# Kernel optimization log

Hardware: AMD Instinct MI355X
Metric: run time of the kernel (lower is better)

The kernel has to match this reference:

```python
import jax, jax.numpy as jnp
import numpy as np

B, N, K = 64, 4096, 16
DIN, DOUT, HID, T = 256, 256, 512, 3
LN_EPS = 1e-5


def _ln2d(x, w, b):
    # LayerNorm over last TWO dims (matches nn.LayerNorm([n_feat, dim]))
    m = jnp.mean(x, axis=(-2, -1), keepdims=True)
    v = jnp.mean(jnp.square(x - m), axis=(-2, -1), keepdims=True)
    return (x - m) * jax.lax.rsqrt(v + LN_EPS) * w + b


def setup_inputs() -> dict:
    key = jax.random.key(0)
    ks = jax.random.split(key, 24)
    s = lambda fan_in: 1.0 / np.sqrt(fan_in)
    d = {
        "inputs": jax.random.normal(ks[0], (B, N, DIN), jnp.float32),
        "slots_init": jax.random.normal(ks[1], (B, K, DOUT), jnp.float32),
        "mu": jax.random.normal(ks[2], (1, 1, DOUT), jnp.float32),
        "logsigma": jax.random.normal(ks[3], (1, 1, DOUT), jnp.float32) * 0.1,
        "ln0_w": jnp.ones((N, DIN), jnp.float32),
        "ln0_b": jnp.zeros((N, DIN), jnp.float32),
        "ln1_w": jnp.ones((K, DOUT), jnp.float32),
        "ln1_b": jnp.zeros((K, DOUT), jnp.float32),
        "ln2_w": jnp.ones((K, DOUT), jnp.float32),
        "ln2_b": jnp.zeros((K, DOUT), jnp.float32),
        "qW": jax.random.uniform(ks[4], (T, DOUT, DOUT), jnp.float32, -s(DOUT), s(DOUT)),
        "qb": jax.random.uniform(ks[5], (T, DOUT), jnp.float32, -s(DOUT), s(DOUT)),
        "kW": jax.random.uniform(ks[6], (T, DOUT, DIN), jnp.float32, -s(DIN), s(DIN)),
        "kb": jax.random.uniform(ks[7], (T, DOUT), jnp.float32, -s(DIN), s(DIN)),
        "vW": jax.random.uniform(ks[8], (T, DOUT, DIN), jnp.float32, -s(DIN), s(DIN)),
        "vb": jax.random.uniform(ks[9], (T, DOUT), jnp.float32, -s(DIN), s(DIN)),
        "m1W": jax.random.uniform(ks[10], (T, HID, DOUT), jnp.float32, -s(DOUT), s(DOUT)),
        "m1b": jax.random.uniform(ks[11], (T, HID), jnp.float32, -s(DOUT), s(DOUT)),
        "m2W": jax.random.uniform(ks[12], (T, DOUT, HID), jnp.float32, -s(HID), s(HID)),
        "m2b": jax.random.uniform(ks[13], (T, DOUT), jnp.float32, -s(HID), s(HID)),
    }
    return d


def reference(inputs, slots_init, mu, logsigma, ln0_w, ln0_b, ln1_w, ln1_b,
              ln2_w, ln2_b, qW, qb, kW, kb, vW, vb, m1W, m1b, m2W, m2b):
    slots = mu + jnp.exp(logsigma) * slots_init          # [B,K,DOUT]
    x = _ln2d(inputs, ln0_w, ln0_b)                      # [B,N,DIN]
    for it in range(T):
        s = _ln2d(slots, ln1_w, ln1_b)
        q = jnp.einsum('bkd,ed->bke', s, qW[it]) + qb[it]     # [B,K,DOUT]
        k = jnp.einsum('bnd,ed->bne', x, kW[it]) + kb[it]     # [B,N,DOUT]
        v = jnp.einsum('bnd,ed->bne', x, vW[it]) + vb[it]     # [B,N,DOUT]
        dist = jnp.einsum('bkd,bnd->bkn', q, k) / K           # note: /out_num_features
        attns = jax.nn.softmax(dist, axis=1)                  # softmax over SLOT dim
        weights = attns / (jnp.sum(attns, axis=-1, keepdims=True) + 1e-7)
        slots = jnp.einsum('bkn,bnd->bkd', weights, v)        # [B,K,DOUT]
        h = _ln2d(slots, ln2_w, ln2_b)
        h = jax.nn.relu(jnp.einsum('bkd,hd->bkh', h, m1W[it]) + m1b[it])
        slots = slots + jnp.einsum('bkh,dh->bkd', h, m2W[it]) + m2b[it]
    return slots
```

## Files before the change

### kernel.cpp

```cpp
#include <hip/hip_runtime.h>
#include <hip/hip_bf16.h>

#define LN_EPS 1e-5f

typedef __attribute__((ext_vector_type(8))) short short8;
typedef __attribute__((ext_vector_type(4))) float f32x4;

__device__ __forceinline__ ushort f2bf(float f) {
    __hip_bfloat16 h = __float2bfloat16(f);
    return *reinterpret_cast<ushort*>(&h);
}
__device__ __forceinline__ float bf2f(ushort u) {
    union { float f; unsigned int i; } c; c.i = ((unsigned int)u) << 16; return c.f;
}

__global__ void kinit(const float* __restrict__ slots_init, const float* __restrict__ mu,
                      const float* __restrict__ logsig, float* __restrict__ slots,
                      float* __restrict__ sums) {
    int i = blockIdx.x * 256 + threadIdx.x;
    int d = i & 255;
    slots[i] = mu[d] + __expf(logsig[d]) * slots_init[i];
    if (blockIdx.x == 0 && threadIdx.x < 128) sums[threadIdx.x] = 0.f;
}

__global__ void ktrans(const float* __restrict__ qW, const float* __restrict__ kW,
                       const float* __restrict__ m1W, const float* __restrict__ m2W,
                       const float* __restrict__ vW,
                       ushort* __restrict__ qWc, ushort* __restrict__ kWT,
                       ushort* __restrict__ m1Wc, ushort* __restrict__ m2Wc,
                       ushort* __restrict__ vWc) {
    int blk = blockIdx.x, t = threadIdx.x;
    int col = t & 63, rq = t >> 6;
    if (blk < 288) {
        const float* src; ushort* dst; int C, tr, tc;
        if (blk < 48)        { int it = blk >> 4, rem = blk & 15; C = 256; tr = rem >> 2; tc = rem & 3;
                               src = qW + it * 65536;  dst = qWc + it * 65536; }
        else if (blk < 96)   { int li = blk - 48; int it = li >> 4, rem = li & 15; C = 256; tr = rem >> 2; tc = rem & 3;
                               src = vW + it * 65536;  dst = vWc + it * 65536; }
        else if (blk < 192)  { int li = blk - 96; int it = li >> 5, rem = li & 31; C = 256; tr = rem >> 2; tc = rem & 3;
                               src = m1W + it * 131072; dst = m1Wc + it * 131072; }
        else                 { int li = blk - 192; int it = li >> 5, rem = li & 31; C = 512; tr = rem >> 3; tc = rem & 7;
                               src = m2W + it * 131072; dst = m2Wc + it * 131072; }
        #pragma unroll
        for (int r = 0; r < 16; r++) {
            int row = r * 4 + rq;
            int idx = (tr * 64 + row) * C + tc * 64 + col;
            dst[idx] = f2bf(src[idx]);
        }
        return;
    }
    __shared__ float tile[64][65];
    int li = blk - 288; int it = li >> 4, rem = li & 15;
    int tr = rem >> 2, tc = rem & 3;
    const float* src = kW + it * 65536; ushort* dst = kWT + it * 65536;
    #pragma unroll
    for (int r = 0; r < 16; r++) {
        int row = r * 4 + rq;
        tile[row][col] = src[(tr * 64 + row) * 256 + tc * 64 + col];
    }
    __syncthreads();
    #pragma unroll
    for (int r = 0; r < 16; r++) {
        int row = r * 4 + rq;
        dst[(tc * 64 + row) * 256 + tr * 64 + col] = f2bf(tile[col][row]);
    }
}

__global__ void l0a(const float* __restrict__ inp, float* __restrict__ sums) {
    int b = blockIdx.x >> 5, seg = blockIdx.x & 31;
    const float4* p = (const float4*)inp + (size_t)b * 262144 + seg * 8192 + threadIdx.x;
    float s = 0.f, sq = 0.f;
    #pragma unroll
    for (int k = 0; k < 32; k++) {
        float4 v = p[k * 256];
        s  += v.x + v.y + v.z + v.w;
        sq += v.x * v.x + v.y * v.y + v.z * v.z + v.w * v.w;
    }
    __shared__ float r1[256], r2[256];
    r1[threadIdx.x] = s; r2[threadIdx.x] = sq; __syncthreads();
    for (int st = 128; st > 0; st >>= 1) {
        if (threadIdx.x < st) { r1[threadIdx.x] += r1[threadIdx.x + st]; r2[threadIdx.x] += r2[threadIdx.x + st]; }
        __syncthreads();
    }
    if (threadIdx.x == 0) { atomicAdd(&sums[b], r1[0]); atomicAdd(&sums[64 + b], r2[0]); }
}

__global__ void l0bs(const float* __restrict__ inp, const float* __restrict__ ln0w,
                     const float* __restrict__ ln0b, const float* __restrict__ sums,
                     ushort* __restrict__ xgs) {
    int gw = blockIdx.x * 4 + (threadIdx.x >> 6);
    int lane = threadIdx.x & 63, l15 = lane & 15, quad = lane >> 4;
    int ntile = gw >> 4;
    int ds = (gw >> 1) & 7;
    int b0 = (gw & 1) * 32;
    int n = ntile * 16 + l15;
    int dcol = ds * 32 + quad * 8;
    const float4* wp = (const float4*)(ln0w + n * 256 + dcol);
    const float4* bp = (const float4*)(ln0b + n * 256 + dcol);
    float4 w0 = wp[0], w1 = wp[1];
    float4 c0 = bp[0], c1 = bp[1];
    #pragma unroll 4
    for (int bi = 0; bi < 32; bi++) {
        int b = b0 + bi;
        float mean = sums[b] * (1.f / 1048576.f);
        float rstd = rsqrtf(sums[64 + b] * (1.f / 1048576.f) - mean * mean + LN_EPS);
        const float4* xp = (const float4*)(inp + (size_t)b * 1048576 + n * 256 + dcol);
        float4 v0 = xp[0], v1 = xp[1];
        ushort o[8];
        o[0] = f2bf((v0.x - mean) * rstd * w0.x + c0.x);
        o[1] = f2bf((v0.y - mean) * rstd * w0.y + c0.y);
        o[2] = f2bf((v0.z - mean) * rstd * w0.z + c0.z);
        o[3] = f2bf((v0.w - mean) * rstd * w0.w + c0.w);
        o[4] = f2bf((v1.x - mean) * rstd * w1.x + c1.x);
        o[5] = f2bf((v1.y - mean) * rstd * w1.y + c1.y);
        o[6] = f2bf((v1.z - mean) * rstd * w1.z + c1.z);
        o[7] = f2bf((v1.w - mean) * rstd * w1.w + c1.w);
        *(short8*)(xgs + ((size_t)((b * 256 + ntile) * 8 + ds) * 64 + lane) * 8) = *(short8*)o;
    }
}

__global__ void kqm(const float* __restrict__ slots, const float* __restrict__ ln1w,
                    const float* __restrict__ ln1b, const ushort* __restrict__ qWc,
                    const float* __restrict__ qb, const ushort* __restrict__ kWT,
                    const float* __restrict__ kb,
                    ushort* __restrict__ qkf, float* __restrict__ qkb,
                    float* __restrict__ denom) {
    int b = blockIdx.x, t = threadIdx.x;
    int lane = t & 63, w = t >> 6, l15 = lane & 15, quad = lane >> 4;
    __shared__ ushort slb[16 * 264];
    __shared__ ushort qsb[16 * 264];
    __shared__ ushort qkl[16 * 264];
    __shared__ float  qsf[16 * 260];
    __shared__ float  r1[256], r2[256];

    const float* sp = slots + b * 4096;
    float vals[16]; float s = 0.f, sq = 0.f;
    #pragma unroll
    for (int k = 0; k < 16; k++) { float v = sp[k * 256 + t]; vals[k] = v; s += v; sq += v * v; }
    r1[t] = s; r2[t] = sq; __syncthreads();
    for (int st = 128; st > 0; st >>= 1) {
        if (t < st) { r1[t] += r1[t + st]; r2[t] += r2[t + st]; }
        __syncthreads();
    }
    float m  = r1[0] * (1.f / 4096.f);
    float rs = rsqrtf(r2[0] * (1.f / 4096.f) - m * m + LN_EPS);
    #pragma unroll
    for (int k = 0; k < 16; k++)
        slb[k * 264 + t] = f2bf((vals[k] - m) * rs * ln1w[k * 256 + t] + ln1b[k * 256 + t]);
    __syncthreads();

    short8 af[8];
    #pragma unroll
    for (int ds = 0; ds < 8; ds++)
        af[ds] = *(const short8*)(&slb[l15 * 264 + ds * 32 + quad * 8]);
    #pragma unroll
    for (int p = 0; p < 4; p++) {
        int et = w * 4 + p;
        f32x4 c = f32x4{0.f, 0.f, 0.f, 0.f};
        #pragma unroll
        for (int ds = 0; ds < 8; ds++) {
            short8 bf_ = *(const short8*)(qWc + (size_t)(et * 16 + l15) * 256 + ds * 32 + quad * 8);
            c = __builtin_amdgcn_mfma_f32_16x16x32_bf16(af[ds], bf_, c, 0, 0, 0);
        }
        float qbv = qb[et * 16 + l15];
        #pragma unroll
        for (int r = 0; r < 4; r++) {
            float val = (c[r] + qbv) * (1.f / 16.f);
            qsf[(quad * 4 + r) * 260 + et * 16 + l15] = val;
            qsb[(quad * 4 + r) * 264 + et * 16 + l15] = f2bf(val);
        }
    }
    __syncthreads();

    {
        int ss = w * 4 + quad;
        float pp = 0.f;
        #pragma unroll
        for (int e = 0; e < 16; e++) pp += qsf[ss * 260 + l15 * 16 + e] * kb[l15 * 16 + e];
        pp += __shfl_xor(pp, 1); pp += __shfl_xor(pp, 2);
        pp += __shfl_xor(pp, 4); pp += __shfl_xor(pp, 8);
        if (l15 == 0) qkb[b * 16 + ss] = pp;
    }
    if (t < 16) denom[b * 16 + t] = 0.f;

    short8 af2[8];
    #pragma unroll
    for (int es = 0; es < 8; es++)
        af2[es] = *(const short8*)(&qsb[l15 * 264 + es * 32 + quad * 8]);
    #pragma unroll
    for (int p = 0; p < 4; p++) {
        int dt = w * 4 + p;
        f32x4 c2 = f32x4{0.f, 0.f, 0.f, 0.f};
        #pragma unroll
        for (int es = 0; es < 8; es++) {
            short8 bf2 = *(const short8*)(kWT + (size_t)(dt * 16 + l15) * 256 + es * 32 + quad * 8);
            c2 = __builtin_amdgcn_mfma_f32_16x16x32_bf16(af2[es], bf2, c2, 0, 0, 0);
        }
        #pragma unroll
        for (int r = 0; r < 4; r++)
            qkl[(quad * 4 + r) * 264 + dt * 16 + l15] = f2bf(c2[r]);
    }
    __syncthreads();

    #pragma unroll
    for (int i = 0; i < 2; i++) {
        int ds = w * 2 + i;
        short8 v = *(const short8*)(&qkl[l15 * 264 + ds * 32 + quad * 8]);
        *(short8*)(qkf + (size_t)(b * 8 + ds) * 512 + lane * 8) = v;
    }
}

__launch_bounds__(256, 4)
__global__ void katt(const ushort* __restrict__ xgs, const ushort* __restrict__ qkf,
                     const float* __restrict__ qkb, float* __restrict__ denom,
                     float* __restrict__ partials) {
    int b = blockIdx.x >> 4, chunk = blockIdx.x & 15;
    int tid = threadIdx.x;
    int lane = tid & 63, w = tid >> 6;
    int l15 = lane & 15, quad = lane >> 4;

    __shared__ ushort xtT[16384];
    __shared__ ushort attn[16 * 72];

    short8 ilo, ihi;
    #pragma unroll
    for (int j = 0; j < 8; j++) {
        ilo[j] = (short)((quad * 8 + j == l15)      ? 0x3F80 : 0);
        ihi[j] = (short)((quad * 8 + j == l15 + 16) ? 0x3F80 : 0);
    }
    int wbase = (w >> 1) * 512 + ((w * 2 + (quad >> 1)) & 3) * 128 + l15 * 8 + (quad & 1) * 4;

    short8 qkfr[8];
    #pragma unroll
    for (int ds = 0; ds < 8; ds++)
        qkfr[ds] = *(const short8*)(qkf + ((size_t)(b * 8 + ds) * 512 + lane * 8));
    float4 qo = *(const float4*)(qkb + b * 16 + quad * 4);

    f32x4 pacc[4];
    #pragma unroll
    for (int u = 0; u < 4; u++) pacc[u] = f32x4{0.f, 0.f, 0.f, 0.f};
    float dp0 = 0.f, dp1 = 0.f, dp2 = 0.f, dp3 = 0.f;

    int tile0 = b * 256 + chunk * 16;

    short8 pf[8];
    #pragma unroll
    for (int i = 0; i < 8; i++)
        pf[i] = *(const short8*)(xgs + (((size_t)(tile0 + w) * 8 + i) * 64 + lane) * 8);

    #pragma unroll 1
    for (int sub = 0; sub < 4; sub++) {
        __syncthreads();
        f32x4 dc = f32x4{0.f, 0.f, 0.f, 0.f};
        #pragma unroll
        for (int ds = 0; ds < 8; ds++)
            dc = __builtin_amdgcn_mfma_f32_16x16x32_bf16(qkfr[ds], pf[ds], dc, 0, 0, 0);
        dc[0] += qo.x; dc[1] += qo.y; dc[2] += qo.z; dc[3] += qo.w;
        float mx = fmaxf(fmaxf(dc[0], dc[1]), fmaxf(dc[2], dc[3]));
        mx = fmaxf(mx, __shfl_xor(mx, 16));
        mx = fmaxf(mx, __shfl_xor(mx, 32));
        float e0 = __expf(dc[0] - mx), e1 = __expf(dc[1] - mx);
        float e2 = __expf(dc[2] - mx), e3 = __expf(dc[3] - mx);
        float lsum = e0 + e1 + e2 + e3;
        lsum += __shfl_xor(lsum, 16); lsum += __shfl_xor(lsum, 32);
        float inv = 1.f / lsum;
        float p0 = e0 * inv, p1 = e1 * inv, p2 = e2 * inv, p3 = e3 * inv;
        dp0 += p0; dp1 += p1; dp2 += p2; dp3 += p3;
        attn[(quad * 4 + 0) * 72 + w * 16 + l15] = f2bf(p0);
        attn[(quad * 4 + 1) * 72 + w * 16 + l15] = f2bf(p1);
        attn[(quad * 4 + 2) * 72 + w * 16 + l15] = f2bf(p2);
        attn[(quad * 4 + 3) * 72 + w * 16 + l15] = f2bf(p3);
        f32x4 zz = f32x4{0.f, 0.f, 0.f, 0.f};
        #pragma unroll
        for (int ds = 0; ds < 8; ds++) {
            f32x4 tlo = __builtin_amdgcn_mfma_f32_16x16x32_bf16(pf[ds], ilo, zz, 0, 0, 0);
            f32x4 thi = __builtin_amdgcn_mfma_f32_16x16x32_bf16(pf[ds], ihi, zz, 0, 0, 0);
            unsigned lo0 = (__float_as_uint(tlo[0]) >> 16) | (__float_as_uint(tlo[1]) & 0xFFFF0000u);
            unsigned lo1 = (__float_as_uint(tlo[2]) >> 16) | (__float_as_uint(tlo[3]) & 0xFFFF0000u);
            unsigned hi0 = (__float_as_uint(thi[0]) >> 16) | (__float_as_uint(thi[1]) & 0xFFFF0000u);
            unsigned hi1 = (__float_as_uint(thi[2]) >> 16) | (__float_as_uint(thi[3]) & 0xFFFF0000u);
            *(uint2*)(&xtT[(ds * 2 + 0) * 1024 + wbase]) = make_uint2(lo0, lo1);
            *(uint2*)(&xtT[(ds * 2 + 1) * 1024 + wbase]) = make_uint2(hi0, hi1);
        }
        if (sub < 3) {
            #pragma unroll
            for (int i = 0; i < 8; i++)
                pf[i] = *(const short8*)(xgs + (((size_t)(tile0 + (sub + 1) * 4 + w) * 8 + i) * 64 + lane) * 8);
        }
        __syncthreads();

        #pragma unroll
        for (int ns = 0; ns < 2; ns++) {
            short8 aa = *(const short8*)(&attn[l15 * 72 + ns * 32 + quad * 8]);
            #pragma unroll
            for (int u = 0; u < 4; u++) {
                short8 bb = *(const short8*)(&xtT[((w * 4 + u) * 2 + ns) * 512 + lane * 8]);
                pacc[u] = __builtin_amdgcn_mfma_f32_16x16x32_bf16(aa, bb, pacc[u], 0, 0, 0);
            }
        }
    }

    #pragma unroll
    for (int m = 1; m < 16; m <<= 1) {
        dp0 += __shfl_xor(dp0, m); dp1 += __shfl_xor(dp1, m);
        dp2 += __shfl_xor(dp2, m); dp3 += __shfl_xor(dp3, m);
    }
    if (l15 == 0) {
        atomicAdd(&denom[b * 16 + quad * 4 + 0], dp0);
        atomicAdd(&denom[b * 16 + quad * 4 + 1], dp1);
        atomicAdd(&denom[b * 16 + quad * 4 + 2], dp2);
        atomicAdd(&denom[b * 16 + quad * 4 + 3], dp3);
    }

    float* pout = partials + (size_t)(b * 16 + chunk) * 4096;
    #pragma unroll
    for (int u = 0; u < 4; u++)
        #pragma unroll
        for (int r = 0; r < 4; r++)
            pout[(quad * 4 + r) * 256 + (w * 4 + u) * 16 + l15] = pacc[u][r];
}

__global__ void ktail(const float* __restrict__ partials, const float* __restrict__ denom,
                      const ushort* __restrict__ vWc, const float* __restrict__ vb,
                      const float* __restrict__ ln2w, const float* __restrict__ ln2b,
                      const ushort* __restrict__ m1Wc, const float* __restrict__ m1b,
                      const ushort* __restrict__ m2Wc, const float* __restrict__ m2b,
                      float* __restrict__ final_out, int write_final,
                      const float* __restrict__ ln1w, const float* __restrict__ ln1b,
                      const ushort* __restrict__ qWc_n, const float* __restrict__ qb_n,
                      const ushort* __restrict__ kWT_n, const float* __restrict__ kb_n,
                      ushort* __restrict__ qkf, float* __restrict__ qkb,
                      float* __restrict__ denom_out, int gen) {
    int b = blockIdx.x, t = threadIdx.x;
    int lane = t & 63, w = t >> 6, l15 = lane & 15, quad = lane >> 4;

    __shared__ char pool[60416];
    __shared__ float dnb[16];
    ushort* axsb = (ushort*)pool;
    ushort* s2b  = (ushort*)(pool + 8448);
    float*  slt  = (float*)(pool + 16896);
    float*  r1   = (float*)(pool + 33280);
    float*  r2   = (float*)(pool + 34304);
    ushort* hlb  = (ushort*)(pool + 35328);
    float*  slt2 = (float*)pool;
    ushort* slbq = (ushort*)(pool + 16896);
    ushort* qkl  = (ushort*)(pool + 16896);
    float*  qsf  = (float*)(pool + 35328);
    ushort* qsb  = (ushort*)(pool + 51968);

    const float* pp = partials + (size_t)b * 65536;
    #pragma unroll
    for (int i = 0; i < 16; i++) {
        float ss = 0.f;
        #pragma unroll
        for (int c = 0; c < 16; c++) ss += pp[c * 4096 + i * 256 + t];
        axsb[i * 264 + t] = f2bf(ss);
    }
    if (t < 16) dnb[t] = denom[b * 16 + t];
    __syncthreads();

    float myv[16];
    {
        short8 af[8];
        #pragma unroll
        for (int ds = 0; ds < 8; ds++)
            af[ds] = *(const short8*)(&axsb[l15 * 264 + ds * 32 + quad * 8]);
        #pragma unroll
        for (int u = 0; u < 4; u++) {
            int et = w * 4 + u;
            f32x4 c = f32x4{0.f, 0.f, 0.f, 0.f};
            #pragma unroll
            for (int ds = 0; ds < 8; ds++) {
                short8 bf_ = *(const short8*)(vWc + (size_t)(et * 16 + l15) * 256 + ds * 32 + quad * 8);
                c = __builtin_amdgcn_mfma_f32_16x16x32_bf16(af[ds], bf_, c, 0, 0, 0);
            }
            float vbe = vb[et * 16 + l15];
            #pragma unroll
            for (int r = 0; r < 4; r++) {
                float A = dnb[quad * 4 + r];
                float val = (c[r] + vbe * A) / (A + 1e-7f);
                slt[(quad * 4 + r) * 256 + et * 16 + l15] = val;
                myv[u * 4 + r] = val;
            }
        }
    }
    {
        float s = 0.f, sq = 0.f;
        #pragma unroll
        for (int i = 0; i < 16; i++) { s += myv[i]; sq += myv[i] * myv[i]; }
        r1[t] = s; r2[t] = sq; __syncthreads();
        for (int st = 128; st > 0; st >>= 1) {
            if (t < st) { r1[t] += r1[t + st]; r2[t] += r2[t + st]; }
            __syncthreads();
        }
    }
    float m2_ = r1[0] * (1.f / 4096.f);
    float rs2 = rsqrtf(r2[0] * (1.f / 4096.f) - m2_ * m2_ + LN_EPS);
    #pragma unroll
    for (int u = 0; u < 4; u++) {
        int e = (w * 4 + u) * 16 + l15;
        #pragma unroll
        for (int r = 0; r < 4; r++) {
            int ss_ = quad * 4 + r;
            s2b[ss_ * 264 + e] = f2bf((myv[u * 4 + r] - m2_) * rs2 * ln2w[ss_ * 256 + e] + ln2b[ss_ * 256 + e]);
        }
    }
    __syncthreads();

    {
        short8 a2[8];
        #pragma unroll
        for (int ds = 0; ds < 8; ds++)
            a2[ds] = *(const short8*)(&s2b[l15 * 264 + ds * 32 + quad * 8]);
        #pragma unroll
        for (int p = 0; p < 8; p++) {
            int jt = w * 8 + p;
            f32x4 c = f32x4{0.f, 0.f, 0.f, 0.f};
            #pragma unroll
            for (int ds = 0; ds < 8; ds++) {
                short8 bf_ = *(const short8*)(m1Wc + (size_t)(jt * 16 + l15) * 256 + ds * 32 + quad * 8);
                c = __builtin_amdgcn_mfma_f32_16x16x32_bf16(a2[ds], bf_, c, 0, 0, 0);
            }
            float bias = m1b[jt * 16 + l15];
            #pragma unroll
            for (int r = 0; r < 4; r++)
                hlb[(quad * 4 + r) * 520 + jt * 16 + l15] = f2bf(fmaxf(c[r] + bias, 0.f));
        }
    }
    __syncthreads();

    {
        short8 a3[16];
        #pragma unroll
        for (int js = 0; js < 16; js++)
            a3[js] = *(const short8*)(&hlb[l15 * 520 + js * 32 + quad * 8]);
        #pragma unroll
        for (int u = 0; u < 4; u++) {
            int dt = w * 4 + u;
            f32x4 c = f32x4{0.f, 0.f, 0.f, 0.f};
            #pragma unroll
            for (int js = 0; js < 16; js++) {
                short8 bf_ = *(const short8*)(m2Wc + (size_t)(dt * 16 + l15) * 512 + js * 32 + quad * 8);
                c = __builtin_amdgcn_mfma_f32_16x16x32_bf16(a3[js], bf_, c, 0, 0, 0);
            }
            float b2 = m2b[dt * 16 + l15];
            #pragma unroll
            for (int r = 0; r < 4; r++) {
                int ss_ = quad * 4 + r, d = dt * 16 + l15;
                float val = slt[ss_ * 256 + d] + c[r] + b2;
                slt2[ss_ * 256 + d] = val;
                if (write_final) final_out[(size_t)b * 4096 + ss_ * 256 + d] = val;
            }
        }
    }
    __syncthreads();

    if (gen) {
        float vals[16]; float s = 0.f, sq = 0.f;
        #pragma unroll
        for (int k = 0; k < 16; k++) { float v = slt2[k * 256 + t]; vals[k] = v; s += v; sq += v * v; }
        r1[t] = s; r2[t] = sq; __syncthreads();
        for (int st = 128; st > 0; st >>= 1) {
            if (t < st) { r1[t] += r1[t + st]; r2[t] += r2[t + st]; }
            __syncthreads();
        }
        float m1_ = r1[0] * (1.f / 4096.f);
        float rs1 = rsqrtf(r2[0] * (1.f / 4096.f) - m1_ * m1_ + LN_EPS);
        #pragma unroll
        for (int k = 0; k < 16; k++)
            slbq[k * 264 + t] = f2bf((vals[k] - m1_) * rs1 * ln1w[k * 256 + t] + ln1b[k * 256 + t]);
        __syncthreads();

        short8 aq[8];
        #pragma unroll
        for (int ds = 0; ds < 8; ds++)
            aq[ds] = *(const short8*)(&slbq[l15 * 264 + ds * 32 + quad * 8]);
        #pragma unroll
        for (int p = 0; p < 4; p++) {
            int et = w * 4 + p;
            f32x4 c = f32x4{0.f, 0.f, 0.f, 0.f};
            #pragma unroll
            for (int ds = 0; ds < 8; ds++) {
                short8 bf_ = *(const short8*)(qWc_n + (size_t)(et * 16 + l15) * 256 + ds * 32 + quad * 8);
                c = __builtin_amdgcn_mfma_f32_16x16x32_bf16(aq[ds], bf_, c, 0, 0, 0);
            }
            float qbv = qb_n[et * 16 + l15];
            #pragma unroll
            for (int r = 0; r < 4; r++) {
                float val = (c[r] + qbv) * (1.f / 16.f);
                qsf[(quad * 4 + r) * 260 + et * 16 + l15] = val;
                qsb[(quad * 4 + r) * 264 + et * 16 + l15] = f2bf(val);
            }
        }
        __syncthreads();

        {
            int ss = w * 4 + quad;
            float pp2 = 0.f;
            #pragma unroll
            for (int e = 0; e < 16; e++) pp2 += qsf[ss * 260 + l15 * 16 + e] * kb_n[l15 * 16 + e];
            pp2 += __shfl_xor(pp2, 1); pp2 += __shfl_xor(pp2, 2);
            pp2 += __shfl_xor(pp2, 4); pp2 += __shfl_xor(pp2, 8);
            if (l15 == 0) qkb[b * 16 + ss] = pp2;
        }
        if (t < 16) denom_out[b * 16 + t] = 0.f;

        short8 aq2[8];
        #pragma unroll
        for (int es = 0; es < 8; es++)
            aq2[es] = *(const short8*)(&qsb[l15 * 264 + es * 32 + quad * 8]);
        #pragma unroll
        for (int p = 0; p < 4; p++) {
            int dt = w * 4 + p;
            f32x4 c2 = f32x4{0.f, 0.f, 0.f, 0.f};
            #pragma unroll
            for (int es = 0; es < 8; es++) {
                short8 bf2 = *(const short8*)(kWT_n + (size_t)(dt * 16 + l15) * 256 + es * 32 + quad * 8);
                c2 = __builtin_amdgcn_mfma_f32_16x16x32_bf16(aq2[es], bf2, c2, 0, 0, 0);
            }
            #pragma unroll
            for (int r = 0; r < 4; r++)
                qkl[(quad * 4 + r) * 264 + dt * 16 + l15] = f2bf(c2[r]);
        }
        __syncthreads();

        #pragma unroll
        for (int i = 0; i < 2; i++) {
            int ds = w * 2 + i;
            short8 v = *(const short8*)(&qkl[l15 * 264 + ds * 32 + quad * 8]);
            *(short8*)(qkf + (size_t)(b * 8 + ds) * 512 + lane * 8) = v;
        }
    }
}

extern "C" void kernel_launch(void* const* d_in, const int* in_sizes, int n_in,
                              void* d_out, int out_size, void* d_ws, size_t ws_size,
                              hipStream_t stream) {
    const float* inputs     = (const float*)d_in[0];
    const float* slots_init = (const float*)d_in[1];
    const float* mu         = (const float*)d_in[2];
    const float* logsig     = (const float*)d_in[3];
    const float* ln0w       = (const float*)d_in[4];
    const float* ln0b       = (const float*)d_in[5];
    const float* ln1w       = (const float*)d_in[6];
    const float* ln1b       = (const float*)d_in[7];
    const float* ln2w       = (const float*)d_in[8];
    const float* ln2b       = (const float*)d_in[9];
    const float* qW         = (const float*)d_in[10];
    const float* qb         = (const float*)d_in[11];
    const float* kW         = (const float*)d_in[12];
    const float* kb         = (const float*)d_in[13];
    const float* vW         = (const float*)d_in[14];
    const float* vb         = (const float*)d_in[15];
    const float* m1W        = (const float*)d_in[16];
    const float* m1b        = (const float*)d_in[17];
    const float* m2W        = (const float*)d_in[18];
    const float* m2b        = (const float*)d_in[19];

    char* ws = (char*)d_ws;
    ushort* xgs     = (ushort*)(ws);
    float*  partials= (float*)(ws + 134217728);
    ushort* qkf     = (ushort*)(ws + 150994944);
    float*  slots   = (float*)(ws + 152567808);
    ushort* qWc     = (ushort*)(ws + 153616384);
    ushort* m1Wc    = (ushort*)(ws + 154009600);
    ushort* m2Wc    = (ushort*)(ws + 154796032);
    ushort* vWc     = (ushort*)(ws + 155582464);
    float*  denom   = (float*)(ws + 155975680);
    float*  qkb     = (float*)(ws + 155979776);
    float*  sums    = (float*)(ws + 155983872);
    ushort* kWT     = (ushort*)(ws + 155984384);

    kinit<<<1024, 256, 0, stream>>>(slots_init, mu, logsig, slots, sums);
    ktrans<<<336, 256, 0, stream>>>(qW, kW, m1W, m2W, vW, qWc, kWT, m1Wc, m2Wc, vWc);
    l0a<<<2048, 256, 0, stream>>>(inputs, sums);
    l0bs<<<1024, 256, 0, stream>>>(inputs, ln0w, ln0b, sums, xgs);
    kqm<<<64, 256, 0, stream>>>(slots, ln1w, ln1b, qWc, qb, kWT, kb, qkf, qkb, denom);

    for (int it = 0; it < 3; it++) {
        katt<<<1024, 256, 0, stream>>>(xgs, qkf, qkb, denom, partials);
        int nx = (it < 2) ? it + 1 : 2;
        ktail<<<64, 256, 0, stream>>>(partials, denom,
                                      vWc + it * 65536, vb + it * 256, ln2w, ln2b,
                                      m1Wc + it * 131072, m1b + it * 512,
                                      m2Wc + it * 131072, m2b + it * 256,
                                      (float*)d_out, it == 2 ? 1 : 0,
                                      ln1w, ln1b,
                                      qWc + nx * 65536, qb + nx * 256,
                                      kWT + nx * 65536, kb + nx * 256,
                                      qkf, qkb, denom, it < 2 ? 1 : 0);
    }
}
```

Before: 384.4 us.

## Widen kqm and ktail to 1024 threads and use shuffle reductions

The per-batch small kernels (kqm, ktail) go from 256 to 1024 threads per block, so each of the 16 waves computes one 16-column MFMA tile instead of four. The LayerNorm reductions switch from a serial shared-memory tree to wave shuffle reductions followed by a 16-entry combine. The q/k generation code is moved into a shared helper. The aim is to cut the latency of these 64-block serial stages, which leave most of the GPU idle, at the cost of higher per-block register and scheduling pressure.

```diff
diff --git a/kernel.cpp b/kernel.cpp
--- a/kernel.cpp
+++ b/kernel.cpp
@@ -119,6 +119,66 @@
     }
 }
 
+__device__ __forceinline__ void qgen_core(
+        int b, int t, int lane, int w, int l15, int quad,
+        ushort* slbq, float* qsf, ushort* qsb, ushort* qkl,
+        const ushort* __restrict__ qWc, const float* __restrict__ qb,
+        const ushort* __restrict__ kWT, const float* __restrict__ kb,
+        ushort* __restrict__ qkf, float* __restrict__ qkb,
+        float* __restrict__ denom_out) {
+    {
+        short8 aq[8];
+        #pragma unroll
+        for (int ds = 0; ds < 8; ds++)
+            aq[ds] = *(const short8*)(&slbq[l15 * 264 + ds * 32 + quad * 8]);
+        int et = w;
+        f32x4 c = f32x4{0.f, 0.f, 0.f, 0.f};
+        #pragma unroll
+        for (int ds = 0; ds < 8; ds++) {
+            short8 bf_ = *(const short8*)(qWc + (size_t)(et * 16 + l15) * 256 + ds * 32 + quad * 8);
+            c = __builtin_amdgcn_mfma_f32_16x16x32_bf16(aq[ds], bf_, c, 0, 0, 0);
+        }
+        float qbv = qb[et * 16 + l15];
+        #pragma unroll
+        for (int r = 0; r < 4; r++) {
+            float val = (c[r] + qbv) * (1.f / 16.f);
+            qsf[(quad * 4 + r) * 260 + et * 16 + l15] = val;
+            qsb[(quad * 4 + r) * 264 + et * 16 + l15] = f2bf(val);
+        }
+    }
+    __syncthreads();
+    {
+        float pp = 0.f;
+        #pragma unroll
+        for (int e = 0; e < 16; e++) pp += qsf[w * 260 + l15 * 16 + e] * kb[l15 * 16 + e];
+        pp += __shfl_xor(pp, 1); pp += __shfl_xor(pp, 2);
+        pp += __shfl_xor(pp, 4); pp += __shfl_xor(pp, 8);
+        if (lane == 0) qkb[b * 16 + w] = pp;
+    }
+    if (t < 16) denom_out[b * 16 + t] = 0.f;
+    {
+        short8 aq2[8];
+        #pragma unroll
+        for (int es = 0; es < 8; es++)
+            aq2[es] = *(const short8*)(&qsb[l15 * 264 + es * 32 + quad * 8]);
+        int dt = w;
+        f32x4 c2 = f32x4{0.f, 0.f, 0.f, 0.f};
+        #pragma unroll
+        for (int es = 0; es < 8; es++) {
+            short8 bf2 = *(const short8*)(kWT + (size_t)(dt * 16 + l15) * 256 + es * 32 + quad * 8);
+            c2 = __builtin_amdgcn_mfma_f32_16x16x32_bf16(aq2[es], bf2, c2, 0, 0, 0);
+        }
+        #pragma unroll
+        for (int r = 0; r < 4; r++)
+            qkl[(quad * 4 + r) * 264 + dt * 16 + l15] = f2bf(c2[r]);
+    }
+    __syncthreads();
+    if (w < 8) {
+        short8 v = *(const short8*)(&qkl[l15 * 264 + w * 32 + quad * 8]);
+        *(short8*)(qkf + (size_t)(b * 8 + w) * 512 + lane * 8) = v;
+    }
+}
+
 __global__ void kqm(const float* __restrict__ slots, const float* __restrict__ ln1w,
                     const float* __restrict__ ln1b, const ushort* __restrict__ qWc,
                     const float* __restrict__ qb, const ushort* __restrict__ kWT,
@@ -127,87 +187,36 @@
                     float* __restrict__ denom) {
     int b = blockIdx.x, t = threadIdx.x;
     int lane = t & 63, w = t >> 6, l15 = lane & 15, quad = lane >> 4;
-    __shared__ ushort slb[16 * 264];
+    __shared__ ushort slbq[16 * 264];
     __shared__ ushort qsb[16 * 264];
     __shared__ ushort qkl[16 * 264];
     __shared__ float  qsf[16 * 260];
-    __shared__ float  r1[256], r2[256];
-
-    const float* sp = slots + b * 4096;
-    float vals[16]; float s = 0.f, sq = 0.f;
-    #pragma unroll
-    for (int k = 0; k < 16; k++) { float v = sp[k * 256 + t]; vals[k] = v; s += v; sq += v * v; }
-    r1[t] = s; r2[t] = sq; __syncthreads();
-    for (int st = 128; st > 0; st >>= 1) {
-        if (t < st) { r1[t] += r1[t + st]; r2[t] += r2[t + st]; }
-        __syncthreads();
-    }
-    float m  = r1[0] * (1.f / 4096.f);
-    float rs = rsqrtf(r2[0] * (1.f / 4096.f) - m * m + LN_EPS);
-    #pragma unroll
-    for (int k = 0; k < 16; k++)
-        slb[k * 264 + t] = f2bf((vals[k] - m) * rs * ln1w[k * 256 + t] + ln1b[k * 256 + t]);
-    __syncthreads();
-
-    short8 af[8];
-    #pragma unroll
-    for (int ds = 0; ds < 8; ds++)
-        af[ds] = *(const short8*)(&slb[l15 * 264 + ds * 32 + quad * 8]);
-    #pragma unroll
-    for (int p = 0; p < 4; p++) {
-        int et = w * 4 + p;
-        f32x4 c = f32x4{0.f, 0.f, 0.f, 0.f};
-        #pragma unroll
-        for (int ds = 0; ds < 8; ds++) {
-            short8 bf_ = *(const short8*)(qWc + (size_t)(et * 16 + l15) * 256 + ds * 32 + quad * 8);
-            c = __builtin_amdgcn_mfma_f32_16x16x32_bf16(af[ds], bf_, c, 0, 0, 0);
-        }
-        float qbv = qb[et * 16 + l15];
-        #pragma unroll
-        for (int r = 0; r < 4; r++) {
-            float val = (c[r] + qbv) * (1.f / 16.f);
-            qsf[(quad * 4 + r) * 260 + et * 16 + l15] = val;
-            qsb[(quad * 4 + r) * 264 + et * 16 + l15] = f2bf(val);
-        }
-    }
-    __syncthreads();
-
-    {
-        int ss = w * 4 + quad;
-        float pp = 0.f;
-        #pragma unroll
-        for (int e = 0; e < 16; e++) pp += qsf[ss * 260 + l15 * 16 + e] * kb[l15 * 16 + e];
-        pp += __shfl_xor(pp, 1); pp += __shfl_xor(pp, 2);
-        pp += __shfl_xor(pp, 4); pp += __shfl_xor(pp, 8);
-        if (l15 == 0) qkb[b * 16 + ss] = pp;
-    }
-    if (t < 16) denom[b * 16 + t] = 0.f;
-
-    short8 af2[8];
-    #pragma unroll
-    for (int es = 0; es < 8; es++)
-        af2[es] = *(const short8*)(&qsb[l15 * 264 + es * 32 + quad * 8]);
-    #pragma unroll
-    for (int p = 0; p < 4; p++) {
-        int dt = w * 4 + p;
-        f32x4 c2 = f32x4{0.f, 0.f, 0.f, 0.f};
-        #pragma unroll
-        for (int es = 0; es < 8; es++) {
-            short8 bf2 = *(const short8*)(kWT + (size_t)(dt * 16 + l15) * 256 + es * 32 + quad * 8);
-            c2 = __builtin_amdgcn_mfma_f32_16x16x32_bf16(af2[es], bf2, c2, 0, 0, 0);
-        }
-        #pragma unroll
-        for (int r = 0; r < 4; r++)
-            qkl[(quad * 4 + r) * 264 + dt * 16 + l15] = f2bf(c2[r]);
-    }
-    __syncthreads();
-
-    #pragma unroll
-    for (int i = 0; i < 2; i++) {
-        int ds = w * 2 + i;
-        short8 v = *(const short8*)(&qkl[l15 * 264 + ds * 32 + quad * 8]);
-        *(short8*)(qkf + (size_t)(b * 8 + ds) * 512 + lane * 8) = v;
-    }
+    __shared__ float  wr1[16], wr2[16];
+
+    int g = t >> 8, c = t & 255;
+    float vals[4]; float s = 0.f, sq = 0.f;
+    #pragma unroll
+    for (int kk = 0; kk < 4; kk++) {
+        float v = slots[b * 4096 + (g * 4 + kk) * 256 + c];
+        vals[kk] = v; s += v; sq += v * v;
+    }
+    #pragma unroll
+    for (int m = 1; m < 64; m <<= 1) { s += __shfl_xor(s, m); sq += __shfl_xor(sq, m); }
+    if (lane == 0) { wr1[w] = s; wr2[w] = sq; }
+    __syncthreads();
+    float ts = 0.f, tsq = 0.f;
+    #pragma unroll
+    for (int i = 0; i < 16; i++) { ts += wr1[i]; tsq += wr2[i]; }
+    float m_  = ts * (1.f / 4096.f);
+    float rs_ = rsqrtf(tsq * (1.f / 4096.f) - m_ * m_ + LN_EPS);
+    #pragma unroll
+    for (int kk = 0; kk < 4; kk++) {
+        int k = g * 4 + kk;
+        slbq[k * 264 + c] = f2bf((vals[kk] - m_) * rs_ * ln1w[k * 256 + c] + ln1b[k * 256 + c]);
+    }
+    __syncthreads();
+    qgen_core(b, t, lane, w, l15, quad, slbq, qsf, qsb, qkl,
+              qWc, qb, kWT, kb, qkf, qkb, denom);
 }
 
 __launch_bounds__(256, 4)
@@ -336,11 +345,10 @@
 
     __shared__ char pool[60416];
     __shared__ float dnb[16];
+    __shared__ float wr1[16], wr2[16];
     ushort* axsb = (ushort*)pool;
     ushort* s2b  = (ushort*)(pool + 8448);
     float*  slt  = (float*)(pool + 16896);
-    float*  r1   = (float*)(pool + 33280);
-    float*  r2   = (float*)(pool + 34304);
     ushort* hlb  = (ushort*)(pool + 35328);
     float*  slt2 = (float*)pool;
     ushort* slbq = (ushort*)(pool + 16896);
@@ -350,59 +358,57 @@
 
     const float* pp = partials + (size_t)b * 65536;
     #pragma unroll
-    for (int i = 0; i < 16; i++) {
+    for (int i = 0; i < 4; i++) {
+        int idx = i * 1024 + t;
         float ss = 0.f;
         #pragma unroll
-        for (int c = 0; c < 16; c++) ss += pp[c * 4096 + i * 256 + t];
-        axsb[i * 264 + t] = f2bf(ss);
+        for (int c = 0; c < 16; c++) ss += pp[c * 4096 + idx];
+        axsb[(idx >> 8) * 264 + (idx & 255)] = f2bf(ss);
     }
     if (t < 16) dnb[t] = denom[b * 16 + t];
     __syncthreads();
 
-    float myv[16];
+    float myv[4];
     {
         short8 af[8];
         #pragma unroll
         for (int ds = 0; ds < 8; ds++)
             af[ds] = *(const short8*)(&axsb[l15 * 264 + ds * 32 + quad * 8]);
-        #pragma unroll
-        for (int u = 0; u < 4; u++) {
-            int et = w * 4 + u;
-            f32x4 c = f32x4{0.f, 0.f, 0.f, 0.f};
-            #pragma unroll
-            for (int ds = 0; ds < 8; ds++) {
-                short8 bf_ = *(const short8*)(vWc + (size_t)(et * 16 + l15) * 256 + ds * 32 + quad * 8);
-                c = __builtin_amdgcn_mfma_f32_16x16x32_bf16(af[ds], bf_, c, 0, 0, 0);
-            }
-            float vbe = vb[et * 16 + l15];
-            #pragma unroll
-            for (int r = 0; r < 4; r++) {
-                float A = dnb[quad * 4 + r];
-                float val = (c[r] + vbe * A) / (A + 1e-7f);
-                slt[(quad * 4 + r) * 256 + et * 16 + l15] = val;
-                myv[u * 4 + r] = val;
-            }
-        }
-    }
-    {
-        float s = 0.f, sq = 0.f;
-        #pragma unroll
-        for (int i = 0; i < 16; i++) { s += myv[i]; sq += myv[i] * myv[i]; }
-        r1[t] = s; r2[t] = sq; __syncthreads();
-        for (int st = 128; st > 0; st >>= 1) {
-            if (t < st) { r1[t] += r1[t + st]; r2[t] += r2[t + st]; }
-            __syncthreads();
-        }
-    }
-    float m2_ = r1[0] * (1.f / 4096.f);
-    float rs2 = rsqrtf(r2[0] * (1.f / 4096.f) - m2_ * m2_ + LN_EPS);
-    #pragma unroll
-    for (int u = 0; u < 4; u++) {
-        int e = (w * 4 + u) * 16 + l15;
+        int et = w;
+        f32x4 c = f32x4{0.f, 0.f, 0.f, 0.f};
+        #pragma unroll
+        for (int ds = 0; ds < 8; ds++) {
+            short8 bf_ = *(const short8*)(vWc + (size_t)(et * 16 + l15) * 256 + ds * 32 + quad * 8);
+            c = __builtin_amdgcn_mfma_f32_16x16x32_bf16(af[ds], bf_, c, 0, 0, 0);
+        }
+        float vbe = vb[et * 16 + l15];
+        #pragma unroll
+        for (int r = 0; r < 4; r++) {
+            float A = dnb[quad * 4 + r];
+            float val = (c[r] + vbe * A) / (A + 1e-7f);
+            slt[(quad * 4 + r) * 256 + et * 16 + l15] = val;
+            myv[r] = val;
+        }
+    }
+    {
+        float s = myv[0] + myv[1] + myv[2] + myv[3];
+        float sq = myv[0]*myv[0] + myv[1]*myv[1] + myv[2]*myv[2] + myv[3]*myv[3];
+        #pragma unroll
+        for (int m = 1; m < 64; m <<= 1) { s += __shfl_xor(s, m); sq += __shfl_xor(sq, m); }
+        if (lane == 0) { wr1[w] = s; wr2[w] = sq; }
+        __syncthreads();
+    }
+    float ts = 0.f, tsq = 0.f;
+    #pragma unroll
+    for (int i = 0; i < 16; i++) { ts += wr1[i]; tsq += wr2[i]; }
+    float m2_ = ts * (1.f / 4096.f);
+    float rs2 = rsqrtf(tsq * (1.f / 4096.f) - m2_ * m2_ + LN_EPS);
+    {
+        int e = w * 16 + l15;
         #pragma unroll
         for (int r = 0; r < 4; r++) {
             int ss_ = quad * 4 + r;
-            s2b[ss_ * 264 + e] = f2bf((myv[u * 4 + r] - m2_) * rs2 * ln2w[ss_ * 256 + e] + ln2b[ss_ * 256 + e]);
+            s2b[ss_ * 264 + e] = f2bf((myv[r] - m2_) * rs2 * ln2w[ss_ * 256 + e] + ln2b[ss_ * 256 + e]);
         }
     }
     __syncthreads();
@@ -413,8 +419,8 @@
         for (int ds = 0; ds < 8; ds++)
             a2[ds] = *(const short8*)(&s2b[l15 * 264 + ds * 32 + quad * 8]);
         #pragma unroll
-        for (int p = 0; p < 8; p++) {
-            int jt = w * 8 + p;
+        for (int p = 0; p < 2; p++) {
+            int jt = w + p * 16;
             f32x4 c = f32x4{0.f, 0.f, 0.f, 0.f};
             #pragma unroll
             for (int ds = 0; ds < 8; ds++) {
@@ -434,102 +440,49 @@
         #pragma unroll
         for (int js = 0; js < 16; js++)
             a3[js] = *(const short8*)(&hlb[l15 * 520 + js * 32 + quad * 8]);
-        #pragma unroll
-        for (int u = 0; u < 4; u++) {
-            int dt = w * 4 + u;
-            f32x4 c = f32x4{0.f, 0.f, 0.f, 0.f};
-            #pragma unroll
-            for (int js = 0; js < 16; js++) {
-                short8 bf_ = *(const short8*)(m2Wc + (size_t)(dt * 16 + l15) * 512 + js * 32 + quad * 8);
-                c = __builtin_amdgcn_mfma_f32_16x16x32_bf16(a3[js], bf_, c, 0, 0, 0);
-            }
-            float b2 = m2b[dt * 16 + l15];
-            #pragma unroll
-            for (int r = 0; r < 4; r++) {
-                int ss_ = quad * 4 + r, d = dt * 16 + l15;
-                float val = slt[ss_ * 256 + d] + c[r] + b2;
-                slt2[ss_ * 256 + d] = val;
-                if (write_final) final_out[(size_t)b * 4096 + ss_ * 256 + d] = val;
-            }
+        int dt = w;
+        f32x4 c = f32x4{0.f, 0.f, 0.f, 0.f};
+        #pragma unroll
+        for (int js = 0; js < 16; js++) {
+            short8 bf_ = *(const short8*)(m2Wc + (size_t)(dt * 16 + l15) * 512 + js * 32 + quad * 8);
+            c = __builtin_amdgcn_mfma_f32_16x16x32_bf16(a3[js], bf_, c, 0, 0, 0);
+        }
+        float b2 = m2b[dt * 16 + l15];
+        #pragma unroll
+        for (int r = 0; r < 4; r++) {
+            int ss_ = quad * 4 + r, d = dt * 16 + l15;
+            float val = slt[ss_ * 256 + d] + c[r] + b2;
+            slt2[ss_ * 256 + d] = val;
+            if (write_final) final_out[(size_t)b * 4096 + ss_ * 256 + d] = val;
         }
     }
     __syncthreads();
 
     if (gen) {
-        float vals[16]; float s = 0.f, sq = 0.f;
-        #pragma unroll
-        for (int k = 0; k < 16; k++) { float v = slt2[k * 256 + t]; vals[k] = v; s += v; sq += v * v; }
-        r1[t] = s; r2[t] = sq; __syncthreads();
-        for (int st = 128; st > 0; st >>= 1) {
-            if (t < st) { r1[t] += r1[t + st]; r2[t] += r2[t + st]; }
-            __syncthreads();
-        }
-        float m1_ = r1[0] * (1.f / 4096.f);
-        float rs1 = rsqrtf(r2[0] * (1.f / 4096.f) - m1_ * m1_ + LN_EPS);
-        #pragma unroll
-        for (int k = 0; k < 16; k++)
-            slbq[k * 264 + t] = f2bf((vals[k] - m1_) * rs1 * ln1w[k * 256 + t] + ln1b[k * 256 + t]);
+        int g = t >> 8, cc = t & 255;
+        float vals[4]; float s = 0.f, sq = 0.f;
+        #pragma unroll
+        for (int kk = 0; kk < 4; kk++) {
+            float v = slt2[(g * 4 + kk) * 256 + cc];
+            vals[kk] = v; s += v; sq += v * v;
+        }
+        #pragma unroll
+        for (int m = 1; m < 64; m <<= 1) { s += __shfl_xor(s, m); sq += __shfl_xor(sq, m); }
+        if (lane == 0) { wr1[w] = s; wr2[w] = sq; }
         __syncthreads();
-
-        short8 aq[8];
-        #pragma unroll
-        for (int ds = 0; ds < 8; ds++)
-            aq[ds] = *(const short8*)(&slbq[l15 * 264 + ds * 32 + quad * 8]);
-        #pragma unroll
-        for (int p = 0; p < 4; p++) {
-            int et = w * 4 + p;
-            f32x4 c = f32x4{0.f, 0.f, 0.f, 0.f};
-            #pragma unroll
-            for (int ds = 0; ds < 8; ds++) {
-                short8 bf_ = *(const short8*)(qWc_n + (size_t)(et * 16 + l15) * 256 + ds * 32 + quad * 8);
-                c = __builtin_amdgcn_mfma_f32_16x16x32_bf16(aq[ds], bf_, c, 0, 0, 0);
-            }
-            float qbv = qb_n[et * 16 + l15];
-            #pragma unroll
-            for (int r = 0; r < 4; r++) {
-                float val = (c[r] + qbv) * (1.f / 16.f);
-                qsf[(quad * 4 + r) * 260 + et * 16 + l15] = val;
-                qsb[(quad * 4 + r) * 264 + et * 16 + l15] = f2bf(val);
-            }
+        float ts1 = 0.f, tsq1 = 0.f;
+        #pragma unroll
+        for (int i = 0; i < 16; i++) { ts1 += wr1[i]; tsq1 += wr2[i]; }
+        float m1_ = ts1 * (1.f / 4096.f);
+        float rs1 = rsqrtf(tsq1 * (1.f / 4096.f) - m1_ * m1_ + LN_EPS);
+        #pragma unroll
+        for (int kk = 0; kk < 4; kk++) {
+            int k = g * 4 + kk;
+            slbq[k * 264 + cc] = f2bf((vals[kk] - m1_) * rs1 * ln1w[k * 256 + cc] + ln1b[k * 256 + cc]);
         }
         __syncthreads();
-
-        {
-            int ss = w * 4 + quad;
-            float pp2 = 0.f;
-            #pragma unroll
-            for (int e = 0; e < 16; e++) pp2 += qsf[ss * 260 + l15 * 16 + e] * kb_n[l15 * 16 + e];
-            pp2 += __shfl_xor(pp2, 1); pp2 += __shfl_xor(pp2, 2);
-            pp2 += __shfl_xor(pp2, 4); pp2 += __shfl_xor(pp2, 8);
-            if (l15 == 0) qkb[b * 16 + ss] = pp2;
-        }
-        if (t < 16) denom_out[b * 16 + t] = 0.f;
-
-        short8 aq2[8];
-        #pragma unroll
-        for (int es = 0; es < 8; es++)
-            aq2[es] = *(const short8*)(&qsb[l15 * 264 + es * 32 + quad * 8]);
-        #pragma unroll
-        for (int p = 0; p < 4; p++) {
-            int dt = w * 4 + p;
-            f32x4 c2 = f32x4{0.f, 0.f, 0.f, 0.f};
-            #pragma unroll
-            for (int es = 0; es < 8; es++) {
-                short8 bf2 = *(const short8*)(kWT_n + (size_t)(dt * 16 + l15) * 256 + es * 32 + quad * 8);
-                c2 = __builtin_amdgcn_mfma_f32_16x16x32_bf16(aq2[es], bf2, c2, 0, 0, 0);
-            }
-            #pragma unroll
-            for (int r = 0; r < 4; r++)
-                qkl[(quad * 4 + r) * 264 + dt * 16 + l15] = f2bf(c2[r]);
-        }
-        __syncthreads();
-
-        #pragma unroll
-        for (int i = 0; i < 2; i++) {
-            int ds = w * 2 + i;
-            short8 v = *(const short8*)(&qkl[l15 * 264 + ds * 32 + quad * 8]);
-            *(short8*)(qkf + (size_t)(b * 8 + ds) * 512 + lane * 8) = v;
-        }
+        qgen_core(b, t, lane, w, l15, quad, slbq, qsf, qsb, qkl,
+                  qWc_n, qb_n, kWT_n, kb_n, qkf, qkb, denom_out);
     }
 }
 
@@ -575,19 +528,19 @@
     ktrans<<<336, 256, 0, stream>>>(qW, kW, m1W, m2W, vW, qWc, kWT, m1Wc, m2Wc, vWc);
     l0a<<<2048, 256, 0, stream>>>(inputs, sums);
     l0bs<<<1024, 256, 0, stream>>>(inputs, ln0w, ln0b, sums, xgs);
-    kqm<<<64, 256, 0, stream>>>(slots, ln1w, ln1b, qWc, qb, kWT, kb, qkf, qkb, denom);
+    kqm<<<64, 1024, 0, stream>>>(slots, ln1w, ln1b, qWc, qb, kWT, kb, qkf, qkb, denom);
 
     for (int it = 0; it < 3; it++) {
         katt<<<1024, 256, 0, stream>>>(xgs, qkf, qkb, denom, partials);
         int nx = (it < 2) ? it + 1 : 2;
-        ktail<<<64, 256, 0, stream>>>(partials, denom,
-                                      vWc + it * 65536, vb + it * 256, ln2w, ln2b,
-                                      m1Wc + it * 131072, m1b + it * 512,
-                                      m2Wc + it * 131072, m2b + it * 256,
-                                      (float*)d_out, it == 2 ? 1 : 0,
-                                      ln1w, ln1b,
-                                      qWc + nx * 65536, qb + nx * 256,
-                                      kWT + nx * 65536, kb + nx * 256,
-                                      qkf, qkb, denom, it < 2 ? 1 : 0);
-    }
-}
+        ktail<<<64, 1024, 0, stream>>>(partials, denom,
+                                       vWc + it * 65536, vb + it * 256, ln2w, ln2b,
+                                       m1Wc + it * 131072, m1b + it * 512,
+                                       m2Wc + it * 131072, m2b + it * 256,
+                                       (float*)d_out, it == 2 ? 1 : 0,
+                                       ln1w, ln1b,
+                                       qWc + nx * 65536, qb + nx * 256,
+                                       kWT + nx * 65536, kb + nx * 256,
+                                       qkf, qkb, denom, it < 2 ? 1 : 0);
+    }
+}
```

Result: faster. 328.5 us (-14.5%).
